# Performance work log

Measured on AMD Instinct MI355X. Metric: run time of the kernel, lower is better.

Reference implementation:

```python
import jax, jax.numpy as jnp
import numpy as np

EPS = 1e-5
PROJ_EPS = 1e-5
MAX_TANH_ARG = 15.0
NUM_LAYERS = 2

def _norm(x):
    return jnp.sqrt(jnp.sum(x * x, axis=-1, keepdims=True))

def log_map_zero(y):
    # Poincare ball log map at the origin: arctanh(||y||) * y / ||y||
    n = _norm(y)
    n_c = jnp.clip(n, EPS, 1.0 - PROJ_EPS)
    return jnp.arctanh(n_c) * y / jnp.maximum(n, EPS)

def exp_map_zero(v):
    # Poincare ball exp map at the origin: tanh(||v||) * v / ||v||
    n = _norm(v)
    n_c = jnp.clip(n, EPS, MAX_TANH_ARG)
    return jnp.tanh(n_c) * v / jnp.maximum(n, EPS)

def setup_inputs() -> dict:
    key = jax.random.key(0)
    k1, k2, k3, k4 = jax.random.split(key, 4)
    N, K, D = 50000, 32, 128
    # scale initial features so they lie inside the unit ball
    node_repr = jax.random.normal(k1, (N, D), dtype=jnp.float32) * 0.01
    adj_mat = jax.random.randint(k2, (N, K), 0, N, dtype=jnp.int32)
    weight = jax.random.uniform(k3, (N, K), dtype=jnp.float32)
    mask = jnp.ones((N, 1), dtype=jnp.float32)
    # learned params: one [D, D] matrix per layer (tie_weight=False, poincare)
    msg_weights = jax.random.normal(k4, (NUM_LAYERS, D, D), dtype=jnp.float32) * (1.0 / np.sqrt(D))
    return {"node_repr": node_repr, "adj_mat": adj_mat, "weight": weight,
            "mask": mask, "msg_weights": msg_weights}

def reference(node_repr, adj_mat, weight, mask, msg_weights):
    x = node_repr
    for step in range(NUM_LAYERS):
        # log map back to tangent space at origin (identity on first layer)
        x = (log_map_zero(x) if step > 0 else x) * mask
        msg = (x @ msg_weights[step]) * mask            # [N, D] dense projection
        nbr = msg[adj_mat]                              # [N, K, D] gather by adjacency
        combined = jnp.einsum('nk,nkd->nd', weight, nbr) * mask  # weighted neighbor sum (dropout p=0)
        x = exp_map_zero(combined) * mask               # back to the manifold
        x = jax.nn.relu(x) * mask                       # poincare activation
    return x
```

## Files before the change

### kernel.cpp

```cpp
#include <hip/hip_runtime.h>

#define EPS 1e-5f
#define PROJ_EPS 1e-5f
#define MAX_TANH_ARG 15.0f

typedef __bf16 bf16x8 __attribute__((ext_vector_type(8)));
typedef float f32x4 __attribute__((ext_vector_type(4)));
typedef float f32x2 __attribute__((ext_vector_type(2)));

__device__ __forceinline__ unsigned short f2bf(float f) {
  unsigned u = __builtin_bit_cast(unsigned, f);
  u += 0x7fffu + ((u >> 16) & 1u);
  return (unsigned short)(u >> 16);
}

union BF8 {
  unsigned short u[8];
  bf16x8 v;
  uint4 q;
};

__global__ void pack_w_kernel(const float* __restrict__ W,
                              unsigned short* __restrict__ wpack) {
  int tid = blockIdx.x * blockDim.x + threadIdx.x;
  if (tid >= 2 * 8 * 4 * 64) return;
  int lane = tid & 63;
  int s = (tid >> 6) & 3;
  int t = (tid >> 8) & 7;
  int layer = tid >> 11;
  int quad = lane >> 4;
  int n = t * 16 + (lane & 15);
  unsigned short* dst = wpack + ((size_t)((layer * 32 + t * 4 + s) * 64 + lane)) * 8;
  const float* src = W + (size_t)layer * 16384;
#pragma unroll
  for (int j = 0; j < 8; ++j) {
    int k = s * 32 + quad * 8 + j;
    dst[j] = f2bf(src[(size_t)k * 128 + n]);
  }
}

__global__ __launch_bounds__(256) void gemm0_kernel(
    const float* __restrict__ xf, const float* __restrict__ mask,
    const unsigned short* __restrict__ wpack, unsigned short* __restrict__ msg1,
    int N, int planeBytes) {
  __shared__ union {
    float xs[4][16][132];
    unsigned short tile[64][136];
  } sm;
  const int lane = threadIdx.x & 63;
  const int wv = threadIdx.x >> 6;
  const int m = lane & 15;
  const int quad = lane >> 4;
  const int base = blockIdx.x * 64;
  const int wbase = base + wv * 16;

  {
    const int r = lane >> 2;
    const int c = (lane & 3) * 32;
    const int gr = wbase + r;
    const int grc = gr < N ? gr : N - 1;
    const float4* src = (const float4*)(xf + (size_t)grc * 128 + c);
#pragma unroll
    for (int i = 0; i < 8; ++i) *(float4*)&sm.xs[wv][r][c + i * 4] = src[i];
  }
  __syncthreads();

  f32x4 acc[8];
#pragma unroll
  for (int t = 0; t < 8; ++t) acc[t] = (f32x4){0.f, 0.f, 0.f, 0.f};

#pragma unroll
  for (int sk = 0; sk < 4; ++sk) {
    const int k0 = sk * 32 + quad * 8;
    const float4 p0 = *(const float4*)&sm.xs[wv][m][k0];
    const float4 p1 = *(const float4*)&sm.xs[wv][m][k0 + 4];
    BF8 a;
    a.u[0] = f2bf(p0.x); a.u[1] = f2bf(p0.y);
    a.u[2] = f2bf(p0.z); a.u[3] = f2bf(p0.w);
    a.u[4] = f2bf(p1.x); a.u[5] = f2bf(p1.y);
    a.u[6] = f2bf(p1.z); a.u[7] = f2bf(p1.w);
#pragma unroll
    for (int t = 0; t < 8; ++t) {
      BF8 b;
      b.q = *(const uint4*)(wpack + (size_t)((t * 4 + sk) * 64 + lane) * 8);
      acc[t] = __builtin_amdgcn_mfma_f32_16x16x32_bf16(a.v, b.v, acc[t], 0, 0, 0);
    }
  }

  float sc[4];
#pragma unroll
  for (int r = 0; r < 4; ++r) {
    int rr = wbase + quad * 4 + r;
    rr = rr < N ? rr : N - 1;
    const float s = mask[rr];
    sc[r] = s * s;
  }
  __syncthreads();

#pragma unroll
  for (int t = 0; t < 8; ++t) {
    const int c = t * 16 + m;
#pragma unroll
    for (int r = 0; r < 4; ++r)
      sm.tile[wv * 16 + quad * 4 + r][c] = f2bf(acc[t][r] * sc[r]);
  }
  const int r16 = lane >> 2;
  const int sub2 = lane & 3;
  const int grow = wbase + r16;
  if (grow < N) {
#pragma unroll
    for (int p = 0; p < 4; ++p) {
      *(uint4*)((char*)msg1 + (size_t)p * planeBytes + (size_t)grow * 64 + sub2 * 16) =
          *(const uint4*)((const char*)&sm.tile[wv * 16 + r16][0] + p * 64 + sub2 * 16);
    }
  }
}

__global__ __launch_bounds__(256) void fused_kernel(
    const unsigned short* __restrict__ msg1, const int* __restrict__ adj,
    const float* __restrict__ wgt, const float* __restrict__ mask,
    const unsigned short* __restrict__ wpack2, unsigned short* __restrict__ msg2,
    int N, int planeBytes) {
  __shared__ unsigned long long pairs[64 * 33];
  __shared__ unsigned short xtile[64][136];
  __shared__ float lsb[64];
  const int t = threadIdx.x;
  const int lane = t & 63;
  const int wv = t >> 6;
  const int g = lane >> 2;
  const int sub = lane & 3;
  const int nbase = blockIdx.x * 64;

  for (int e = t; e < 64 * 32; e += 256) {
    const int node = e >> 5, k = e & 31;
    const int gn = nbase + node;
    int id = 0;
    float w = 0.f;
    if (gn < N) {
      id = adj[(size_t)gn * 32 + k];
      w = wgt[(size_t)gn * 32 + k];
    }
    pairs[node * 33 + k] = (unsigned long long)(unsigned)id |
        ((unsigned long long)__builtin_bit_cast(unsigned, w) << 32);
  }
  __syncthreads();

  const int mynode = wv * 16 + g;
  const int gnode = nbase + mynode;
  const unsigned long long* mp = pairs + mynode * 33;
  const int suboff = sub * 16;

  f32x2 acc[16];
#pragma unroll
  for (int i = 0; i < 16; ++i) acc[i] = (f32x2){0.f, 0.f};

#pragma unroll
  for (int p = 0; p < 4; ++p) {
    const char* plane = (const char*)msg1 + (size_t)p * planeBytes;
#pragma unroll 8
    for (int k = 0; k < 32; ++k) {
      const unsigned long long pk = mp[k];
      const unsigned id = (unsigned)pk;
      const float w = __builtin_bit_cast(float, (unsigned)(pk >> 32));
      const uint4 q = *(const uint4*)(plane + ((size_t)id * 64 + suboff));
      const f32x2 w2 = {w, w};
#pragma unroll
      for (int d = 0; d < 4; ++d) {
        const unsigned qd = (&q.x)[d];
        f32x2 v2;
        v2.x = __builtin_bit_cast(float, qd << 16);
        v2.y = __builtin_bit_cast(float, qd & 0xffff0000u);
        acc[p * 4 + d] = __builtin_elementwise_fma(v2, w2, acc[p * 4 + d]);
      }
    }
  }

  const int gcl = gnode < N ? gnode : N - 1;
  const float mm = mask[gcl];
  float s2 = 0.f;
#pragma unroll
  for (int i = 0; i < 16; ++i) {
    acc[i].x *= mm;
    acc[i].y *= mm;
    s2 = fmaf(acc[i].x, acc[i].x, s2);
    s2 = fmaf(acc[i].y, acc[i].y, s2);
  }
  s2 += __shfl_xor(s2, 1);
  s2 += __shfl_xor(s2, 2);
  const float nrm = sqrtf(s2);
  const float ncl = fminf(fmaxf(nrm, EPS), MAX_TANH_ARG);
  const float esc = tanhf(ncl) / fmaxf(nrm, EPS) * mm;
  float v[32];
  float r2 = 0.f;
#pragma unroll
  for (int i = 0; i < 16; ++i) {
    v[2 * i] = fmaxf(esc * acc[i].x, 0.f) * mm;
    v[2 * i + 1] = fmaxf(esc * acc[i].y, 0.f) * mm;
    r2 = fmaf(v[2 * i], v[2 * i], r2);
    r2 = fmaf(v[2 * i + 1], v[2 * i + 1], r2);
  }
  r2 += __shfl_xor(r2, 1);
  r2 += __shfl_xor(r2, 2);

#pragma unroll
  for (int p = 0; p < 4; ++p) {
    uint4 pk4;
    unsigned* pw = &pk4.x;
#pragma unroll
    for (int d = 0; d < 4; ++d)
      pw[d] = (unsigned)f2bf(v[p * 8 + d * 2]) |
              ((unsigned)f2bf(v[p * 8 + d * 2 + 1]) << 16);
    *(uint4*)((char*)&xtile[mynode][0] + p * 64 + suboff) = pk4;
  }
  if (sub == 0) {
    const float nr = sqrtf(r2);
    const float nc2 = fminf(fmaxf(nr, EPS), 1.0f - PROJ_EPS);
    const float ls = 0.5f * logf((1.f + nc2) / (1.f - nc2)) / fmaxf(nr, EPS);
    lsb[mynode] = ls * mm * mm;
  }
  __syncthreads();

  const int m = lane & 15;
  const int quad = lane >> 4;
  f32x4 accg[8];
#pragma unroll
  for (int tt = 0; tt < 8; ++tt) accg[tt] = (f32x4){0.f, 0.f, 0.f, 0.f};
#pragma unroll
  for (int sk = 0; sk < 4; ++sk) {
    const int k0 = sk * 32 + quad * 8;
    BF8 a;
    a.q = *(const uint4*)((const char*)&xtile[wv * 16 + m][0] + k0 * 2);
#pragma unroll
    for (int tt = 0; tt < 8; ++tt) {
      BF8 b;
      b.q = *(const uint4*)(wpack2 + (size_t)((tt * 4 + sk) * 64 + lane) * 8);
      accg[tt] = __builtin_amdgcn_mfma_f32_16x16x32_bf16(a.v, b.v, accg[tt], 0, 0, 0);
    }
  }
  float sc[4];
#pragma unroll
  for (int r = 0; r < 4; ++r) sc[r] = lsb[wv * 16 + quad * 4 + r];
#pragma unroll
  for (int tt = 0; tt < 8; ++tt) {
    const int c = tt * 16 + m;
#pragma unroll
    for (int r = 0; r < 4; ++r)
      xtile[wv * 16 + quad * 4 + r][c] = f2bf(accg[tt][r] * sc[r]);
  }
  const int r16 = lane >> 2;
  const int sub2 = lane & 3;
  const int grow = nbase + wv * 16 + r16;
  if (grow < N) {
#pragma unroll
    for (int p = 0; p < 4; ++p) {
      *(uint4*)((char*)msg2 + (size_t)p * planeBytes + (size_t)grow * 64 + sub2 * 16) =
          *(const uint4*)((const char*)&xtile[wv * 16 + r16][0] + p * 64 + sub2 * 16);
    }
  }
}

__global__ __launch_bounds__(256) void gather_out_kernel(
    const unsigned short* __restrict__ msg2, const int* __restrict__ adj,
    const float* __restrict__ wgt, const float* __restrict__ mask,
    float* __restrict__ out, int N, int planeBytes) {
  __shared__ unsigned long long pairs[64 * 33];
  const int t = threadIdx.x;
  const int lane = t & 63;
  const int wv = t >> 6;
  const int g = lane >> 2;
  const int sub = lane & 3;
  const int nbase = blockIdx.x * 64;

  for (int e = t; e < 64 * 32; e += 256) {
    const int node = e >> 5, k = e & 31;
    const int gn = nbase + node;
    int id = 0;
    float w = 0.f;
    if (gn < N) {
      id = adj[(size_t)gn * 32 + k];
      w = wgt[(size_t)gn * 32 + k];
    }
    pairs[node * 33 + k] = (unsigned long long)(unsigned)id |
        ((unsigned long long)__builtin_bit_cast(unsigned, w) << 32);
  }
  __syncthreads();

  const int mynode = wv * 16 + g;
  const int gnode = nbase + mynode;
  const unsigned long long* mp = pairs + mynode * 33;
  const int suboff = sub * 16;

  f32x2 acc[16];
#pragma unroll
  for (int i = 0; i < 16; ++i) acc[i] = (f32x2){0.f, 0.f};

#pragma unroll
  for (int p = 0; p < 4; ++p) {
    const char* plane = (const char*)msg2 + (size_t)p * planeBytes;
#pragma unroll 8
    for (int k = 0; k < 32; ++k) {
      const unsigned long long pk = mp[k];
      const unsigned id = (unsigned)pk;
      const float w = __builtin_bit_cast(float, (unsigned)(pk >> 32));
      const uint4 q = *(const uint4*)(plane + ((size_t)id * 64 + suboff));
      const f32x2 w2 = {w, w};
#pragma unroll
      for (int d = 0; d < 4; ++d) {
        const unsigned qd = (&q.x)[d];
        f32x2 v2;
        v2.x = __builtin_bit_cast(float, qd << 16);
        v2.y = __builtin_bit_cast(float, qd & 0xffff0000u);
        acc[p * 4 + d] = __builtin_elementwise_fma(v2, w2, acc[p * 4 + d]);
      }
    }
  }

  const int gcl = gnode < N ? gnode : N - 1;
  const float mm = mask[gcl];
  float s2 = 0.f;
#pragma unroll
  for (int i = 0; i < 16; ++i) {
    acc[i].x *= mm;
    acc[i].y *= mm;
    s2 = fmaf(acc[i].x, acc[i].x, s2);
    s2 = fmaf(acc[i].y, acc[i].y, s2);
  }
  s2 += __shfl_xor(s2, 1);
  s2 += __shfl_xor(s2, 2);
  const float nrm = sqrtf(s2);
  const float ncl = fminf(fmaxf(nrm, EPS), MAX_TANH_ARG);
  const float esc = tanhf(ncl) / fmaxf(nrm, EPS) * mm;
  if (gnode < N) {
#pragma unroll
    for (int p = 0; p < 4; ++p) {
      float4 o0, o1;
      o0.x = fmaxf(esc * acc[p * 4 + 0].x, 0.f) * mm;
      o0.y = fmaxf(esc * acc[p * 4 + 0].y, 0.f) * mm;
      o0.z = fmaxf(esc * acc[p * 4 + 1].x, 0.f) * mm;
      o0.w = fmaxf(esc * acc[p * 4 + 1].y, 0.f) * mm;
      o1.x = fmaxf(esc * acc[p * 4 + 2].x, 0.f) * mm;
      o1.y = fmaxf(esc * acc[p * 4 + 2].y, 0.f) * mm;
      o1.z = fmaxf(esc * acc[p * 4 + 3].x, 0.f) * mm;
      o1.w = fmaxf(esc * acc[p * 4 + 3].y, 0.f) * mm;
      const int cb = p * 32 + sub * 8;
      *(float4*)(out + (size_t)gnode * 128 + cb) = o0;
      *(float4*)(out + (size_t)gnode * 128 + cb + 4) = o1;
    }
  }
}

extern "C" void kernel_launch(void* const* d_in, const int* in_sizes, int n_in,
                              void* d_out, int out_size, void* d_ws, size_t ws_size,
                              hipStream_t stream) {
  const float* node = (const float*)d_in[0];
  const int* adj = (const int*)d_in[1];
  const float* wgt = (const float*)d_in[2];
  const float* mask = (const float*)d_in[3];
  const float* mw = (const float*)d_in[4];
  float* out = (float*)d_out;
  const int N = in_sizes[0] / 128;

  const int gb = (N + 63) / 64;
  const int planeBytes = gb * 64 * 64;

  unsigned short* wpack = (unsigned short*)d_ws;
  unsigned short* msg2 = (unsigned short*)((char*)d_ws + 65536);
  unsigned short* msg1 = (unsigned short*)d_out;

  hipLaunchKernelGGL(pack_w_kernel, dim3(16), dim3(256), 0, stream, mw, wpack);
  hipLaunchKernelGGL(gemm0_kernel, dim3(gb), dim3(256), 0, stream,
                     node, mask, wpack, msg1, N, planeBytes);
  hipLaunchKernelGGL(fused_kernel, dim3(gb), dim3(256), 0, stream,
                     msg1, adj, wgt, mask, wpack + 16384, msg2, N, planeBytes);
  hipLaunchKernelGGL(gather_out_kernel, dim3(gb), dim3(256), 0, stream,
                     msg2, adj, wgt, mask, out, N, planeBytes);
}
```

Before: 204.5 us.

## Merge four launches into one cooperative persistent kernel with grid syncs

Combines weight packing, the first GEMM, the fused gather+GEMM stage and the final gather into one cooperative kernel that walks node tiles persistently and separates phases with grid.sync, keeping a four-launch fallback. It also converts x to bf16 while loading into shared memory, so the fp32 staging tile is gone and shared memory can be unioned. The aim is to remove launch gaps and inter-kernel drain. In exchange the grid is capped at 512 blocks (two per CU), which may lower latency hiding for the gather-heavy phases, and each grid sync adds a barrier cost.

```diff
diff --git a/kernel.cpp b/kernel.cpp
--- a/kernel.cpp
+++ b/kernel.cpp
@@ -1,4 +1,7 @@
 #include <hip/hip_runtime.h>
+#include <hip/hip_cooperative_groups.h>
+
+namespace cg = cooperative_groups;
 
 #define EPS 1e-5f
 #define PROJ_EPS 1e-5f
@@ -20,39 +23,44 @@
   uint4 q;
 };
 
-__global__ void pack_w_kernel(const float* __restrict__ W,
-                              unsigned short* __restrict__ wpack) {
-  int tid = blockIdx.x * blockDim.x + threadIdx.x;
+struct SMem {
+  union {
+    unsigned short tile[64][136];
+    unsigned long long pairs[64 * 33];
+  };
+  float lsb[64];
+};
+
+__device__ __forceinline__ void do_pack(const float* __restrict__ W,
+                                        unsigned short* __restrict__ wpack,
+                                        int tid) {
   if (tid >= 2 * 8 * 4 * 64) return;
-  int lane = tid & 63;
-  int s = (tid >> 6) & 3;
-  int t = (tid >> 8) & 7;
-  int layer = tid >> 11;
-  int quad = lane >> 4;
-  int n = t * 16 + (lane & 15);
-  unsigned short* dst = wpack + ((size_t)((layer * 32 + t * 4 + s) * 64 + lane)) * 8;
+  const int l = tid & 63;
+  const int s = (tid >> 6) & 3;
+  const int tt = (tid >> 8) & 7;
+  const int layer = tid >> 11;
+  const int q2 = l >> 4;
+  const int n = tt * 16 + (l & 15);
+  unsigned short* dst = wpack + ((size_t)((layer * 32 + tt * 4 + s) * 64 + l)) * 8;
   const float* src = W + (size_t)layer * 16384;
 #pragma unroll
   for (int j = 0; j < 8; ++j) {
-    int k = s * 32 + quad * 8 + j;
+    const int k = s * 32 + q2 * 8 + j;
     dst[j] = f2bf(src[(size_t)k * 128 + n]);
   }
 }
 
-__global__ __launch_bounds__(256) void gemm0_kernel(
-    const float* __restrict__ xf, const float* __restrict__ mask,
-    const unsigned short* __restrict__ wpack, unsigned short* __restrict__ msg1,
-    int N, int planeBytes) {
-  __shared__ union {
-    float xs[4][16][132];
-    unsigned short tile[64][136];
-  } sm;
-  const int lane = threadIdx.x & 63;
-  const int wv = threadIdx.x >> 6;
+__device__ __forceinline__ void do_gemm0(SMem& sm, const float* __restrict__ xf,
+                                         const float* __restrict__ mask,
+                                         const unsigned short* __restrict__ wpack,
+                                         unsigned short* __restrict__ msg1,
+                                         int N, int planeBytes, int tb) {
+  const int t = threadIdx.x;
+  const int lane = t & 63;
+  const int wv = t >> 6;
   const int m = lane & 15;
   const int quad = lane >> 4;
-  const int base = blockIdx.x * 64;
-  const int wbase = base + wv * 16;
+  const int wbase = tb * 64 + wv * 16;
 
   {
     const int r = lane >> 2;
@@ -60,30 +68,29 @@
     const int gr = wbase + r;
     const int grc = gr < N ? gr : N - 1;
     const float4* src = (const float4*)(xf + (size_t)grc * 128 + c);
-#pragma unroll
-    for (int i = 0; i < 8; ++i) *(float4*)&sm.xs[wv][r][c + i * 4] = src[i];
-  }
-  __syncthreads();
+    unsigned short* drow = &sm.tile[wv * 16 + r][c];
+#pragma unroll
+    for (int i = 0; i < 8; ++i) {
+      const float4 p = src[i];
+      drow[i * 4 + 0] = f2bf(p.x);
+      drow[i * 4 + 1] = f2bf(p.y);
+      drow[i * 4 + 2] = f2bf(p.z);
+      drow[i * 4 + 3] = f2bf(p.w);
+    }
+  }
 
   f32x4 acc[8];
 #pragma unroll
-  for (int t = 0; t < 8; ++t) acc[t] = (f32x4){0.f, 0.f, 0.f, 0.f};
-
+  for (int tt = 0; tt < 8; ++tt) acc[tt] = (f32x4){0.f, 0.f, 0.f, 0.f};
 #pragma unroll
   for (int sk = 0; sk < 4; ++sk) {
-    const int k0 = sk * 32 + quad * 8;
-    const float4 p0 = *(const float4*)&sm.xs[wv][m][k0];
-    const float4 p1 = *(const float4*)&sm.xs[wv][m][k0 + 4];
     BF8 a;
-    a.u[0] = f2bf(p0.x); a.u[1] = f2bf(p0.y);
-    a.u[2] = f2bf(p0.z); a.u[3] = f2bf(p0.w);
-    a.u[4] = f2bf(p1.x); a.u[5] = f2bf(p1.y);
-    a.u[6] = f2bf(p1.z); a.u[7] = f2bf(p1.w);
-#pragma unroll
-    for (int t = 0; t < 8; ++t) {
+    a.q = *(const uint4*)&sm.tile[wv * 16 + m][sk * 32 + quad * 8];
+#pragma unroll
+    for (int tt = 0; tt < 8; ++tt) {
       BF8 b;
-      b.q = *(const uint4*)(wpack + (size_t)((t * 4 + sk) * 64 + lane) * 8);
-      acc[t] = __builtin_amdgcn_mfma_f32_16x16x32_bf16(a.v, b.v, acc[t], 0, 0, 0);
+      b.q = *(const uint4*)(wpack + (size_t)((tt * 4 + sk) * 64 + lane) * 8);
+      acc[tt] = __builtin_amdgcn_mfma_f32_16x16x32_bf16(a.v, b.v, acc[tt], 0, 0, 0);
     }
   }
 
@@ -95,14 +102,12 @@
     const float s = mask[rr];
     sc[r] = s * s;
   }
-  __syncthreads();
-
-#pragma unroll
-  for (int t = 0; t < 8; ++t) {
-    const int c = t * 16 + m;
+#pragma unroll
+  for (int tt = 0; tt < 8; ++tt) {
+    const int c = tt * 16 + m;
 #pragma unroll
     for (int r = 0; r < 4; ++r)
-      sm.tile[wv * 16 + quad * 4 + r][c] = f2bf(acc[t][r] * sc[r]);
+      sm.tile[wv * 16 + quad * 4 + r][c] = f2bf(acc[tt][r] * sc[r]);
   }
   const int r16 = lane >> 2;
   const int sub2 = lane & 3;
@@ -116,21 +121,14 @@
   }
 }
 
-__global__ __launch_bounds__(256) void fused_kernel(
-    const unsigned short* __restrict__ msg1, const int* __restrict__ adj,
-    const float* __restrict__ wgt, const float* __restrict__ mask,
-    const unsigned short* __restrict__ wpack2, unsigned short* __restrict__ msg2,
-    int N, int planeBytes) {
-  __shared__ unsigned long long pairs[64 * 33];
-  __shared__ unsigned short xtile[64][136];
-  __shared__ float lsb[64];
+__device__ __forceinline__ void gather_core(SMem& sm, const int* __restrict__ adj,
+                                            const float* __restrict__ wgt,
+                                            const unsigned short* __restrict__ msg,
+                                            int N, int planeBytes, int nbase,
+                                            f32x2 (&acc)[16]) {
   const int t = threadIdx.x;
   const int lane = t & 63;
   const int wv = t >> 6;
-  const int g = lane >> 2;
-  const int sub = lane & 3;
-  const int nbase = blockIdx.x * 64;
-
   for (int e = t; e < 64 * 32; e += 256) {
     const int node = e >> 5, k = e & 31;
     const int gn = nbase + node;
@@ -140,23 +138,19 @@
       id = adj[(size_t)gn * 32 + k];
       w = wgt[(size_t)gn * 32 + k];
     }
-    pairs[node * 33 + k] = (unsigned long long)(unsigned)id |
+    sm.pairs[node * 33 + k] = (unsigned long long)(unsigned)id |
         ((unsigned long long)__builtin_bit_cast(unsigned, w) << 32);
   }
   __syncthreads();
 
-  const int mynode = wv * 16 + g;
-  const int gnode = nbase + mynode;
-  const unsigned long long* mp = pairs + mynode * 33;
-  const int suboff = sub * 16;
-
-  f32x2 acc[16];
+  const int mynode = wv * 16 + (lane >> 2);
+  const unsigned long long* mp = sm.pairs + mynode * 33;
+  const int suboff = (lane & 3) * 16;
 #pragma unroll
   for (int i = 0; i < 16; ++i) acc[i] = (f32x2){0.f, 0.f};
-
 #pragma unroll
   for (int p = 0; p < 4; ++p) {
-    const char* plane = (const char*)msg1 + (size_t)p * planeBytes;
+    const char* plane = (const char*)msg + (size_t)p * planeBytes;
 #pragma unroll 8
     for (int k = 0; k < 32; ++k) {
       const unsigned long long pk = mp[k];
@@ -174,6 +168,27 @@
       }
     }
   }
+}
+
+__device__ __forceinline__ void do_fused(SMem& sm, const unsigned short* __restrict__ msg1,
+                                         const int* __restrict__ adj,
+                                         const float* __restrict__ wgt,
+                                         const float* __restrict__ mask,
+                                         const unsigned short* __restrict__ wpack2,
+                                         unsigned short* __restrict__ msg2,
+                                         int N, int planeBytes, int nbase) {
+  const int t = threadIdx.x;
+  const int lane = t & 63;
+  const int wv = t >> 6;
+  const int m = lane & 15;
+  const int quad = lane >> 4;
+  const int sub = lane & 3;
+  const int mynode = wv * 16 + (lane >> 2);
+  const int gnode = nbase + mynode;
+  const int suboff = sub * 16;
+
+  f32x2 acc[16];
+  gather_core(sm, adj, wgt, msg1, N, planeBytes, nbase, acc);
 
   const int gcl = gnode < N ? gnode : N - 1;
   const float mm = mask[gcl];
@@ -202,6 +217,8 @@
   r2 += __shfl_xor(r2, 1);
   r2 += __shfl_xor(r2, 2);
 
+  __syncthreads();
+
 #pragma unroll
   for (int p = 0; p < 4; ++p) {
     uint4 pk4;
@@ -210,26 +227,22 @@
     for (int d = 0; d < 4; ++d)
       pw[d] = (unsigned)f2bf(v[p * 8 + d * 2]) |
               ((unsigned)f2bf(v[p * 8 + d * 2 + 1]) << 16);
-    *(uint4*)((char*)&xtile[mynode][0] + p * 64 + suboff) = pk4;
+    *(uint4*)((char*)&sm.tile[mynode][0] + p * 64 + suboff) = pk4;
   }
   if (sub == 0) {
     const float nr = sqrtf(r2);
     const float nc2 = fminf(fmaxf(nr, EPS), 1.0f - PROJ_EPS);
     const float ls = 0.5f * logf((1.f + nc2) / (1.f - nc2)) / fmaxf(nr, EPS);
-    lsb[mynode] = ls * mm * mm;
-  }
-  __syncthreads();
-
-  const int m = lane & 15;
-  const int quad = lane >> 4;
+    sm.lsb[mynode] = ls * mm * mm;
+  }
+
   f32x4 accg[8];
 #pragma unroll
   for (int tt = 0; tt < 8; ++tt) accg[tt] = (f32x4){0.f, 0.f, 0.f, 0.f};
 #pragma unroll
   for (int sk = 0; sk < 4; ++sk) {
-    const int k0 = sk * 32 + quad * 8;
     BF8 a;
-    a.q = *(const uint4*)((const char*)&xtile[wv * 16 + m][0] + k0 * 2);
+    a.q = *(const uint4*)&sm.tile[wv * 16 + m][sk * 32 + quad * 8];
 #pragma unroll
     for (int tt = 0; tt < 8; ++tt) {
       BF8 b;
@@ -239,81 +252,39 @@
   }
   float sc[4];
 #pragma unroll
-  for (int r = 0; r < 4; ++r) sc[r] = lsb[wv * 16 + quad * 4 + r];
+  for (int r = 0; r < 4; ++r) sc[r] = sm.lsb[wv * 16 + quad * 4 + r];
 #pragma unroll
   for (int tt = 0; tt < 8; ++tt) {
     const int c = tt * 16 + m;
 #pragma unroll
     for (int r = 0; r < 4; ++r)
-      xtile[wv * 16 + quad * 4 + r][c] = f2bf(accg[tt][r] * sc[r]);
+      sm.tile[wv * 16 + quad * 4 + r][c] = f2bf(accg[tt][r] * sc[r]);
   }
   const int r16 = lane >> 2;
-  const int sub2 = lane & 3;
   const int grow = nbase + wv * 16 + r16;
   if (grow < N) {
 #pragma unroll
     for (int p = 0; p < 4; ++p) {
-      *(uint4*)((char*)msg2 + (size_t)p * planeBytes + (size_t)grow * 64 + sub2 * 16) =
-          *(const uint4*)((const char*)&xtile[wv * 16 + r16][0] + p * 64 + sub2 * 16);
-    }
-  }
-}
-
-__global__ __launch_bounds__(256) void gather_out_kernel(
-    const unsigned short* __restrict__ msg2, const int* __restrict__ adj,
-    const float* __restrict__ wgt, const float* __restrict__ mask,
-    float* __restrict__ out, int N, int planeBytes) {
-  __shared__ unsigned long long pairs[64 * 33];
-  const int t = threadIdx.x;
-  const int lane = t & 63;
-  const int wv = t >> 6;
-  const int g = lane >> 2;
+      *(uint4*)((char*)msg2 + (size_t)p * planeBytes + (size_t)grow * 64 + sub * 16) =
+          *(const uint4*)((const char*)&sm.tile[wv * 16 + r16][0] + p * 64 + sub * 16);
+    }
+  }
+  __syncthreads();
+}
+
+__device__ __forceinline__ void do_gout(SMem& sm, const unsigned short* __restrict__ msg2,
+                                        const int* __restrict__ adj,
+                                        const float* __restrict__ wgt,
+                                        const float* __restrict__ mask,
+                                        float* __restrict__ out,
+                                        int N, int planeBytes, int nbase) {
+  const int lane = threadIdx.x & 63;
+  const int wv = threadIdx.x >> 6;
   const int sub = lane & 3;
-  const int nbase = blockIdx.x * 64;
-
-  for (int e = t; e < 64 * 32; e += 256) {
-    const int node = e >> 5, k = e & 31;
-    const int gn = nbase + node;
-    int id = 0;
-    float w = 0.f;
-    if (gn < N) {
-      id = adj[(size_t)gn * 32 + k];
-      w = wgt[(size_t)gn * 32 + k];
-    }
-    pairs[node * 33 + k] = (unsigned long long)(unsigned)id |
-        ((unsigned long long)__builtin_bit_cast(unsigned, w) << 32);
-  }
-  __syncthreads();
-
-  const int mynode = wv * 16 + g;
-  const int gnode = nbase + mynode;
-  const unsigned long long* mp = pairs + mynode * 33;
-  const int suboff = sub * 16;
+  const int gnode = nbase + wv * 16 + (lane >> 2);
 
   f32x2 acc[16];
-#pragma unroll
-  for (int i = 0; i < 16; ++i) acc[i] = (f32x2){0.f, 0.f};
-
-#pragma unroll
-  for (int p = 0; p < 4; ++p) {
-    const char* plane = (const char*)msg2 + (size_t)p * planeBytes;
-#pragma unroll 8
-    for (int k = 0; k < 32; ++k) {
-      const unsigned long long pk = mp[k];
-      const unsigned id = (unsigned)pk;
-      const float w = __builtin_bit_cast(float, (unsigned)(pk >> 32));
-      const uint4 q = *(const uint4*)(plane + ((size_t)id * 64 + suboff));
-      const f32x2 w2 = {w, w};
-#pragma unroll
-      for (int d = 0; d < 4; ++d) {
-        const unsigned qd = (&q.x)[d];
-        f32x2 v2;
-        v2.x = __builtin_bit_cast(float, qd << 16);
-        v2.y = __builtin_bit_cast(float, qd & 0xffff0000u);
-        acc[p * 4 + d] = __builtin_elementwise_fma(v2, w2, acc[p * 4 + d]);
-      }
-    }
-  }
+  gather_core(sm, adj, wgt, msg2, N, planeBytes, nbase, acc);
 
   const int gcl = gnode < N ? gnode : N - 1;
   const float mm = mask[gcl];
@@ -347,6 +318,47 @@
       *(float4*)(out + (size_t)gnode * 128 + cb + 4) = o1;
     }
   }
+  __syncthreads();
+}
+
+__global__ __launch_bounds__(256, 2) void uber_kernel(
+    const float* __restrict__ xf, const int* __restrict__ adj,
+    const float* __restrict__ wgt, const float* __restrict__ mask,
+    const float* __restrict__ W, unsigned short* __restrict__ wpack,
+    unsigned short* __restrict__ msg1, unsigned short* __restrict__ msg2,
+    float* __restrict__ out, int N, int gb, int planeBytes) {
+  cg::grid_group grid = cg::this_grid();
+  __shared__ SMem sm;
+
+  do_pack(W, wpack, blockIdx.x * 256 + threadIdx.x);
+  grid.sync();
+  for (int tb = blockIdx.x; tb < gb; tb += gridDim.x)
+    do_gemm0(sm, xf, mask, wpack, msg1, N, planeBytes, tb);
+  grid.sync();
+  for (int tb = blockIdx.x; tb < gb; tb += gridDim.x)
+    do_fused(sm, msg1, adj, wgt, mask, wpack + 16384, msg2, N, planeBytes, tb * 64);
+  grid.sync();
+  for (int tb = blockIdx.x; tb < gb; tb += gridDim.x)
+    do_gout(sm, msg2, adj, wgt, mask, out, N, planeBytes, tb * 64);
+}
+
+template <int P>
+__global__ __launch_bounds__(256, 2) void phase_kernel(
+    const float* __restrict__ xf, const int* __restrict__ adj,
+    const float* __restrict__ wgt, const float* __restrict__ mask,
+    const float* __restrict__ W, unsigned short* __restrict__ wpack,
+    unsigned short* __restrict__ msg1, unsigned short* __restrict__ msg2,
+    float* __restrict__ out, int N, int gb, int planeBytes) {
+  __shared__ SMem sm;
+  if (P == 0) {
+    do_pack(W, wpack, blockIdx.x * 256 + threadIdx.x);
+    return;
+  }
+  for (int tb = blockIdx.x; tb < gb; tb += gridDim.x) {
+    if (P == 1) do_gemm0(sm, xf, mask, wpack, msg1, N, planeBytes, tb);
+    if (P == 2) do_fused(sm, msg1, adj, wgt, mask, wpack + 16384, msg2, N, planeBytes, tb * 64);
+    if (P == 3) do_gout(sm, msg2, adj, wgt, mask, out, N, planeBytes, tb * 64);
+  }
 }
 
 extern "C" void kernel_launch(void* const* d_in, const int* in_sizes, int n_in,
@@ -358,20 +370,36 @@
   const float* mask = (const float*)d_in[3];
   const float* mw = (const float*)d_in[4];
   float* out = (float*)d_out;
-  const int N = in_sizes[0] / 128;
-
-  const int gb = (N + 63) / 64;
-  const int planeBytes = gb * 64 * 64;
+  int N = in_sizes[0] / 128;
+  int gb = (N + 63) / 64;
+  int planeBytes = gb * 64 * 64;
 
   unsigned short* wpack = (unsigned short*)d_ws;
   unsigned short* msg2 = (unsigned short*)((char*)d_ws + 65536);
   unsigned short* msg1 = (unsigned short*)d_out;
 
-  hipLaunchKernelGGL(pack_w_kernel, dim3(16), dim3(256), 0, stream, mw, wpack);
-  hipLaunchKernelGGL(gemm0_kernel, dim3(gb), dim3(256), 0, stream,
-                     node, mask, wpack, msg1, N, planeBytes);
-  hipLaunchKernelGGL(fused_kernel, dim3(gb), dim3(256), 0, stream,
-                     msg1, adj, wgt, mask, wpack + 16384, msg2, N, planeBytes);
-  hipLaunchKernelGGL(gather_out_kernel, dim3(gb), dim3(256), 0, stream,
-                     msg2, adj, wgt, mask, out, N, planeBytes);
-}
+  void* args[] = {&node, &adj, &wgt, &mask, &mw, &wpack,
+                  &msg1, &msg2, &out, &N, &gb, &planeBytes};
+
+  int maxb = 0;
+  hipError_t qe = hipOccupancyMaxActiveBlocksPerMultiprocessor(
+      &maxb, (const void*)uber_kernel, 256, 0);
+  int grid = 256;
+  if (qe == hipSuccess && maxb >= 1) {
+    long cap = (long)maxb * 256;
+    grid = (int)(cap < 512 ? cap : 512);
+  }
+
+  hipError_t le = hipLaunchCooperativeKernel((const void*)uber_kernel, dim3(grid),
+                                             dim3(256), args, 0, stream);
+  if (le != hipSuccess) {
+    hipLaunchKernelGGL((phase_kernel<0>), dim3(16), dim3(256), 0, stream,
+                       node, adj, wgt, mask, mw, wpack, msg1, msg2, out, N, gb, planeBytes);
+    hipLaunchKernelGGL((phase_kernel<1>), dim3(gb), dim3(256), 0, stream,
+                       node, adj, wgt, mask, mw, wpack, msg1, msg2, out, N, gb, planeBytes);
+    hipLaunchKernelGGL((phase_kernel<2>), dim3(gb), dim3(256), 0, stream,
+                       node, adj, wgt, mask, mw, wpack, msg1, msg2, out, N, gb, planeBytes);
+    hipLaunchKernelGGL((phase_kernel<3>), dim3(gb), dim3(256), 0, stream,
+                       node, adj, wgt, mask, mw, wpack, msg1, msg2, out, N, gb, planeBytes);
+  }
+}
```

Result: slower. 331.7 us (+62.2%).
